# Kernel optimization log

Measured on AMD Instinct MI355X. Metric: run time of the kernel, lower is better.

## Reference

```python
import jax, jax.numpy as jnp
import numpy as np

D_MODEL = 1024
N_HEADS = 16
D_HEAD = D_MODEL // N_HEADS


def setup_inputs() -> dict:
    key = jax.random.key(0)
    ks = jax.random.split(key, 5)
    scale = 1.0 / np.sqrt(D_MODEL)
    return {
        "x": jax.random.normal(ks[0], (2, 2048, D_MODEL), dtype=jnp.float32),
        "W_q": jax.random.normal(ks[1], (D_MODEL, D_MODEL), dtype=jnp.float32) * scale,
        "W_k": jax.random.normal(ks[2], (D_MODEL, D_MODEL), dtype=jnp.float32) * scale,
        "W_v": jax.random.normal(ks[3], (D_MODEL, D_MODEL), dtype=jnp.float32) * scale,
        "W_o": jax.random.normal(ks[4], (D_MODEL, D_MODEL), dtype=jnp.float32) * scale,
    }


def reference(x, W_q, W_k, W_v, W_o):
    B, S, _ = x.shape
    # nn.Linear computes x @ W.T; weights stored [out, in]
    def proj(W):
        y = jnp.einsum("bsd,ed->bse", x, W)
        return y.reshape(B, S, N_HEADS, D_HEAD).transpose(0, 2, 1, 3)  # [B,H,S,Dh]

    q, k, v = proj(W_q), proj(W_k), proj(W_v)
    scores = jnp.einsum("bhqd,bhkd->bhqk", q, k) / jnp.sqrt(jnp.float32(D_HEAD))
    causal = jnp.triu(jnp.ones((S, S), dtype=bool), k=1)
    scores = jnp.where(causal, -jnp.inf, scores)
    attn = jax.nn.softmax(scores, axis=-1)
    out = jnp.einsum("bhqk,bhkd->bhqd", attn, v)  # [B,H,S,Dh]
    out = out.transpose(0, 2, 1, 3).reshape(B, S, D_MODEL)
    return jnp.einsum("bsd,ed->bse", out, W_o)
```

## Files before the change

### kernel.cpp

```cpp
#include <hip/hip_runtime.h>


#define DMODEL 1024
#define NHEADS 16
#define DHEAD  64
#define SEQ    2048
#define BATCH  2
#define MROWS  (BATCH * SEQ)

typedef __bf16 bf16x8 __attribute__((ext_vector_type(8)));
typedef __bf16 bf16x4 __attribute__((ext_vector_type(4)));
typedef float  f32x4  __attribute__((ext_vector_type(4)));

__device__ __forceinline__ f32x4 mfma16(bf16x8 a, bf16x8 b, f32x4 c) {
    return __builtin_amdgcn_mfma_f32_16x16x32_bf16(a, b, c, 0, 0, 0);
}

__device__ __forceinline__ bf16x8 ld8(const float* p) {
    const f32x4 a0 = *(const f32x4*)p;
    const f32x4 a1 = *(const f32x4*)(p + 4);
    bf16x8 v;
    v[0] = (__bf16)a0[0]; v[1] = (__bf16)a0[1];
    v[2] = (__bf16)a0[2]; v[3] = (__bf16)a0[3];
    v[4] = (__bf16)a1[0]; v[5] = (__bf16)a1[1];
    v[6] = (__bf16)a1[2]; v[7] = (__bf16)a1[3];
    return v;
}

__device__ __forceinline__ void gll16(const __bf16* g, __bf16* l) {
    __builtin_amdgcn_global_load_lds(
        (const __attribute__((address_space(1))) void*)g,
        (__attribute__((address_space(3))) void*)l,
        16, 0, 0);
}

__global__ __launch_bounds__(256) void cvt_kernel(const float* __restrict__ x,
                                                  const float* __restrict__ Wq,
                                                  const float* __restrict__ Wk,
                                                  const float* __restrict__ Wv,
                                                  const float* __restrict__ Wo,
                                                  __bf16* __restrict__ xb,
                                                  __bf16* __restrict__ wcat) {
    const int y = blockIdx.y;
    const float* src;
    __bf16* dst;
    int nchunks;
    if (y == 0) { src = x; dst = xb; nchunks = (MROWS * DMODEL) / 8; }
    else {
        src = (y == 1) ? Wq : (y == 2) ? Wk : (y == 3) ? Wv : Wo;
        dst = wcat + (size_t)(y - 1) * DMODEL * DMODEL;
        nchunks = (DMODEL * DMODEL) / 8;
    }
    const int c = blockIdx.x * 256 + threadIdx.x;
    if (c < nchunks) *(bf16x8*)(dst + (size_t)c * 8) = ld8(src + (size_t)c * 8);
}

template <typename TC>
__device__ __forceinline__ void gemm_bb_body(const __bf16* __restrict__ A,
                                             const __bf16* __restrict__ W,
                                             TC* __restrict__ C,
                                             __bf16* __restrict__ VT,
                                             bool vt, int m0, int n0,
                                             float scale) {
    constexpr int K = DMODEL;
    __shared__ __align__(16) __bf16 As[128][64];
    __shared__ __align__(16) __bf16 Bs[128][64];

    const int tid  = threadIdx.x;
    const int lane = tid & 63;
    const int wave = tid >> 6;
    const int quad = lane >> 4;
    const int l16  = lane & 15;
    const int wm   = wave & 1;
    const int wn   = wave >> 1;

    const int sr = lane >> 3;
    const int sc = ((lane & 7) ^ sr) * 8;

    f32x4 acc[4][4] = {};

    for (int k0 = 0; k0 < K; k0 += 64) {
        __syncthreads();
#pragma unroll
        for (int s = 0; s < 4; ++s) {
            const int row = s * 32 + wave * 8 + sr;
            gll16(A + (size_t)(m0 + row) * K + k0 + sc, &As[s * 32 + wave * 8][0]);
            gll16(W + (size_t)(n0 + row) * K + k0 + sc, &Bs[s * 32 + wave * 8][0]);
        }
        __syncthreads();

#pragma unroll
        for (int h = 0; h < 2; ++h) {
            bf16x8 af[4], bfr[4];
#pragma unroll
            for (int i = 0; i < 4; ++i) {
                const int gr = ((h * 4 + quad) ^ (l16 & 7)) * 8;
                af[i]  = *(const bf16x8*)(&As[wm * 64 + i * 16 + l16][gr]);
                bfr[i] = *(const bf16x8*)(&Bs[wn * 64 + i * 16 + l16][gr]);
            }
#pragma unroll
            for (int mi = 0; mi < 4; ++mi)
#pragma unroll
                for (int ni = 0; ni < 4; ++ni)
                    acc[mi][ni] = mfma16(af[mi], bfr[ni], acc[mi][ni]);
        }
    }

    if (!vt) {
#pragma unroll
        for (int mi = 0; mi < 4; ++mi)
#pragma unroll
            for (int ni = 0; ni < 4; ++ni)
#pragma unroll
                for (int r = 0; r < 4; ++r) {
                    int row = m0 + wm * 64 + mi * 16 + quad * 4 + r;
                    int col = n0 + wn * 64 + ni * 16 + l16;
                    C[(size_t)row * DMODEL + col] = (TC)(acc[mi][ni][r] * scale);
                }
    } else {
#pragma unroll
        for (int mi = 0; mi < 4; ++mi)
#pragma unroll
            for (int ni = 0; ni < 4; ++ni) {
                const int m  = m0 + wm * 64 + mi * 16 + quad * 4;
                const int hd = n0 + wn * 64 + ni * 16 + l16;
                bf16x4 v4;
#pragma unroll
                for (int r = 0; r < 4; ++r) v4[r] = (__bf16)acc[mi][ni][r];
                *(bf16x4*)(VT + (size_t)hd * MROWS + m) = v4;
            }
    }
}

#define QSCALE 0.1803368801111204f

__global__ __launch_bounds__(256) void qkv_kernel(const __bf16* __restrict__ X,
                                                  const __bf16* __restrict__ wcat,
                                                  __bf16* __restrict__ Q,
                                                  __bf16* __restrict__ K,
                                                  __bf16* __restrict__ VT) {
    const int z = blockIdx.z;
    const __bf16* W = wcat + (size_t)z * DMODEL * DMODEL;
    __bf16* Y = (z == 0) ? Q : K;
    const float scale = (z == 0) ? QSCALE : 1.0f;
    gemm_bb_body<__bf16>(X, W, Y, VT, z == 2,
                         blockIdx.y * 128, blockIdx.x * 128, scale);
}

__global__ __launch_bounds__(256) void out_gemm_kernel(const __bf16* __restrict__ A,
                                                       const __bf16* __restrict__ W,
                                                       float* __restrict__ C) {
    gemm_bb_body<float>(A, W, C, nullptr, false,
                        blockIdx.y * 128, blockIdx.x * 128, 1.0f);
}

__global__ __launch_bounds__(128) void attn_kernel(const __bf16* __restrict__ Q,
                                                   const __bf16* __restrict__ Kg,
                                                   const __bf16* __restrict__ VTg,
                                                   __bf16* __restrict__ O) {
    const int bh = blockIdx.x;
    const int qt = 63 - blockIdx.y;
    const int b = bh >> 4, h = bh & 15;
    const size_t base = (size_t)b * SEQ * DMODEL + (size_t)h * DHEAD;

    const int tid  = threadIdx.x;
    const int lane = tid & 63;
    const int wave = tid >> 6;
    const int quad = lane >> 4;
    const int l16  = lane & 15;

    __shared__ __align__(16) __bf16 Ks[32][64];
    __shared__ __align__(16) __bf16 Vs[64][32];
    __shared__ __align__(16) __bf16 Ps[2][16][40];

    const int ksr = lane >> 3;
    const int ksc = ((lane & 7) ^ ksr) * 8;
    const int vsr = lane >> 2;
    const int vsc = ((lane & 3) ^ ((lane >> 3) & 3)) * 8;

    const int qrow = qt * 32 + wave * 16 + l16;

    const bf16x8 qf0 = *(const bf16x8*)(Q + base + (size_t)qrow * DMODEL + quad * 8);
    const bf16x8 qf1 = *(const bf16x8*)(Q + base + (size_t)qrow * DMODEL + 32 + quad * 8);

    f32x4 oacc[4] = {};
    float m_i = -1e30f, l_i = 0.f;

    for (int kt = 0; kt <= qt; ++kt) {
        const int k0 = kt * 32;
        __syncthreads();
#pragma unroll
        for (int j = 0; j < 2; ++j) {
            gll16(Kg + base + (size_t)(k0 + wave * 16 + j * 8 + ksr) * DMODEL + ksc,
                  &Ks[wave * 16 + j * 8][0]);
            gll16(VTg + (size_t)(h * 64 + j * 32 + wave * 16 + vsr) * MROWS
                      + (size_t)b * SEQ + k0 + vsc,
                  &Vs[j * 32 + wave * 16][0]);
        }
        __syncthreads();

        const bool diag = (kt == qt);

        const int g0 = ((quad ^ (l16 & 7))) * 8;
        const int g1 = ((quad ^ 4) ^ (l16 & 7)) * 8;
        const bf16x8 kf00 = *(const bf16x8*)(&Ks[l16][g0]);
        const bf16x8 kf01 = *(const bf16x8*)(&Ks[l16][g1]);
        const bf16x8 kf10 = *(const bf16x8*)(&Ks[16 + l16][g0]);
        const bf16x8 kf11 = *(const bf16x8*)(&Ks[16 + l16][g1]);
        f32x4 s0 = {}, s1 = {};
        s0 = mfma16(kf00, qf0, s0); s0 = mfma16(kf01, qf1, s0);
        s1 = mfma16(kf10, qf0, s1); s1 = mfma16(kf11, qf1, s1);

        float mx;
        bool ok[2][4];
        if (!diag) {
            float m0 = s0[0];
#pragma unroll
            for (int r = 1; r < 4; ++r) m0 = fmaxf(m0, s0[r]);
#pragma unroll
            for (int r = 0; r < 4; ++r) m0 = fmaxf(m0, s1[r]);
            mx = m0;
        } else {
            mx = -1e30f;
#pragma unroll
            for (int hh = 0; hh < 2; ++hh)
#pragma unroll
                for (int r = 0; r < 4; ++r) {
                    const int kk = k0 + hh * 16 + quad * 4 + r;
                    ok[hh][r] = (kk <= qrow);
                    const float v = hh ? s1[r] : s0[r];
                    mx = fmaxf(mx, ok[hh][r] ? v : -1e30f);
                }
        }
        mx = fmaxf(mx, __shfl_xor(mx, 16));
        mx = fmaxf(mx, __shfl_xor(mx, 32));
        const float mnew  = fmaxf(m_i, mx);
        const float alpha = exp2f(m_i - mnew);
        m_i = mnew;

        float p[2][4];
        float rs = 0.f;
        if (!diag) {
#pragma unroll
            for (int hh = 0; hh < 2; ++hh)
#pragma unroll
                for (int r = 0; r < 4; ++r) {
                    p[hh][r] = exp2f((hh ? s1[r] : s0[r]) - mnew);
                    rs += p[hh][r];
                }
        } else {
#pragma unroll
            for (int hh = 0; hh < 2; ++hh)
#pragma unroll
                for (int r = 0; r < 4; ++r) {
                    p[hh][r] = ok[hh][r] ? exp2f((hh ? s1[r] : s0[r]) - mnew) : 0.f;
                    rs += p[hh][r];
                }
        }
        rs += __shfl_xor(rs, 16);
        rs += __shfl_xor(rs, 32);
        l_i = l_i * alpha + rs;

        bf16x4 w0, w1;
#pragma unroll
        for (int r = 0; r < 4; ++r) { w0[r] = (__bf16)p[0][r]; w1[r] = (__bf16)p[1][r]; }
        *(bf16x4*)(&Ps[wave][l16][quad * 4])      = w0;
        *(bf16x4*)(&Ps[wave][l16][16 + quad * 4]) = w1;

        const bf16x8 pf = *(const bf16x8*)(&Ps[wave][l16][quad * 8]);
        const int vg = (quad ^ ((l16 >> 1) & 3)) * 8;
#pragma unroll
        for (int f = 0; f < 4; ++f) {
            const bf16x8 vf = *(const bf16x8*)(&Vs[f * 16 + l16][vg]);
            oacc[f] = mfma16(vf, pf, oacc[f] * alpha);
        }
    }

    const float inv = (l_i > 0.f) ? (1.f / l_i) : 0.f;
#pragma unroll
    for (int f = 0; f < 4; ++f) {
        bf16x4 o;
#pragma unroll
        for (int r = 0; r < 4; ++r) o[r] = (__bf16)(oacc[f][r] * inv);
        *(bf16x4*)(O + base + (size_t)qrow * DMODEL + f * 16 + quad * 4) = o;
    }
}

extern "C" void kernel_launch(void* const* d_in, const int* in_sizes, int n_in,
                              void* d_out, int out_size, void* d_ws, size_t ws_size,
                              hipStream_t stream) {
    const float* x  = (const float*)d_in[0];
    const float* Wq = (const float*)d_in[1];
    const float* Wk = (const float*)d_in[2];
    const float* Wv = (const float*)d_in[3];
    const float* Wo = (const float*)d_in[4];
    float* out = (float*)d_out;

    const size_t tm = (size_t)MROWS * DMODEL;
    const size_t tw = (size_t)DMODEL * DMODEL;
    __bf16* Q    = (__bf16*)d_ws;
    __bf16* K    = Q + tm;
    __bf16* VT   = K + tm;
    __bf16* xb   = VT + tm;
    __bf16* wcat = xb + tm;

    dim3 gc(2048, 5);
    cvt_kernel<<<gc, 256, 0, stream>>>(x, Wq, Wk, Wv, Wo, xb, wcat);

    dim3 g1(DMODEL / 128, MROWS / 128, 3);
    qkv_kernel<<<g1, 256, 0, stream>>>(xb, wcat, Q, K, VT);

    dim3 g2(BATCH * NHEADS, SEQ / 32);
    attn_kernel<<<g2, 128, 0, stream>>>(Q, K, VT, Q);

    dim3 g3(DMODEL / 128, MROWS / 128);
    out_gemm_kernel<<<g3, 256, 0, stream>>>(Q, wcat + 3 * tw, out);
}
```

Baseline: 217.5 us.

## Widen attention KV tile to 64 keys and halve GEMM K-step to 32

The attention kernel now processes 64 keys per iteration using larger swizzled K/V shared tiles and two PV MFMAs per output fragment. This halves the number of loop iterations, barriers and online-softmax rescales per query tile. The projection GEMM drops its K-step from 64 to 32 with a simpler, unswizzled LDS layout. That shrinks shared memory use but doubles barrier count and may add LDS bank conflicts. The diagonal tile now masks up to 64 keys, so more masked work is wasted on even query tiles.

```diff
diff --git a/kernel.cpp b/kernel.cpp
--- a/kernel.cpp
+++ b/kernel.cpp
@@ -63,8 +63,8 @@
                                              bool vt, int m0, int n0,
                                              float scale) {
     constexpr int K = DMODEL;
-    __shared__ __align__(16) __bf16 As[128][64];
-    __shared__ __align__(16) __bf16 Bs[128][64];
+    __shared__ __align__(16) __bf16 As[128][32];
+    __shared__ __align__(16) __bf16 Bs[128][32];
 
     const int tid  = threadIdx.x;
     const int lane = tid & 63;
@@ -74,36 +74,35 @@
     const int wm   = wave & 1;
     const int wn   = wave >> 1;
 
-    const int sr = lane >> 3;
-    const int sc = ((lane & 7) ^ sr) * 8;
+    const int srow = lane >> 2;
+    const int scol = (lane & 3) * 8;
+
+    const __bf16* a0p = A + (size_t)(m0 + wave * 16 + srow) * K + scol;
+    const __bf16* a1p = A + (size_t)(m0 + 64 + wave * 16 + srow) * K + scol;
+    const __bf16* b0p = W + (size_t)(n0 + wave * 16 + srow) * K + scol;
+    const __bf16* b1p = W + (size_t)(n0 + 64 + wave * 16 + srow) * K + scol;
 
     f32x4 acc[4][4] = {};
 
-    for (int k0 = 0; k0 < K; k0 += 64) {
+    for (int k0 = 0; k0 < K; k0 += 32) {
         __syncthreads();
-#pragma unroll
-        for (int s = 0; s < 4; ++s) {
-            const int row = s * 32 + wave * 8 + sr;
-            gll16(A + (size_t)(m0 + row) * K + k0 + sc, &As[s * 32 + wave * 8][0]);
-            gll16(W + (size_t)(n0 + row) * K + k0 + sc, &Bs[s * 32 + wave * 8][0]);
-        }
+        gll16(a0p + k0, &As[wave * 16][0]);
+        gll16(a1p + k0, &As[64 + wave * 16][0]);
+        gll16(b0p + k0, &Bs[wave * 16][0]);
+        gll16(b1p + k0, &Bs[64 + wave * 16][0]);
         __syncthreads();
 
-#pragma unroll
-        for (int h = 0; h < 2; ++h) {
-            bf16x8 af[4], bfr[4];
-#pragma unroll
-            for (int i = 0; i < 4; ++i) {
-                const int gr = ((h * 4 + quad) ^ (l16 & 7)) * 8;
-                af[i]  = *(const bf16x8*)(&As[wm * 64 + i * 16 + l16][gr]);
-                bfr[i] = *(const bf16x8*)(&Bs[wn * 64 + i * 16 + l16][gr]);
-            }
-#pragma unroll
-            for (int mi = 0; mi < 4; ++mi)
-#pragma unroll
-                for (int ni = 0; ni < 4; ++ni)
-                    acc[mi][ni] = mfma16(af[mi], bfr[ni], acc[mi][ni]);
-        }
+        bf16x8 af[4], bfr[4];
+#pragma unroll
+        for (int i = 0; i < 4; ++i) {
+            af[i]  = *(const bf16x8*)(&As[wm * 64 + i * 16 + l16][quad * 8]);
+            bfr[i] = *(const bf16x8*)(&Bs[wn * 64 + i * 16 + l16][quad * 8]);
+        }
+#pragma unroll
+        for (int mi = 0; mi < 4; ++mi)
+#pragma unroll
+            for (int ni = 0; ni < 4; ++ni)
+                acc[mi][ni] = mfma16(af[mi], bfr[ni], acc[mi][ni]);
     }
 
     if (!vt) {
@@ -169,14 +168,12 @@
     const int quad = lane >> 4;
     const int l16  = lane & 15;
 
-    __shared__ __align__(16) __bf16 Ks[32][64];
-    __shared__ __align__(16) __bf16 Vs[64][32];
-    __shared__ __align__(16) __bf16 Ps[2][16][40];
-
-    const int ksr = lane >> 3;
-    const int ksc = ((lane & 7) ^ ksr) * 8;
-    const int vsr = lane >> 2;
-    const int vsc = ((lane & 3) ^ ((lane >> 3) & 3)) * 8;
+    __shared__ __align__(16) __bf16 Ks[64][64];
+    __shared__ __align__(16) __bf16 Vs[64][64];
+    __shared__ __align__(16) __bf16 Ps[2][2][16][40];
+
+    const int sr = lane >> 3;
+    const int sc = ((lane & 7) ^ sr) * 8;
 
     const int qrow = qt * 32 + wave * 16 + l16;
 
@@ -186,50 +183,51 @@
     f32x4 oacc[4] = {};
     float m_i = -1e30f, l_i = 0.f;
 
-    for (int kt = 0; kt <= qt; ++kt) {
-        const int k0 = kt * 32;
+    const int ntiles = (qt >> 1) + 1;
+    const int gsw = (l16 & 7);
+
+    for (int kt = 0; kt < ntiles; ++kt) {
+        const int k0 = kt * 64;
         __syncthreads();
 #pragma unroll
-        for (int j = 0; j < 2; ++j) {
-            gll16(Kg + base + (size_t)(k0 + wave * 16 + j * 8 + ksr) * DMODEL + ksc,
-                  &Ks[wave * 16 + j * 8][0]);
-            gll16(VTg + (size_t)(h * 64 + j * 32 + wave * 16 + vsr) * MROWS
-                      + (size_t)b * SEQ + k0 + vsc,
-                  &Vs[j * 32 + wave * 16][0]);
+        for (int j = 0; j < 4; ++j) {
+            const int row = wave * 32 + j * 8;
+            gll16(Kg + base + (size_t)(k0 + row + sr) * DMODEL + sc, &Ks[row][0]);
+            gll16(VTg + (size_t)(h * 64 + row + sr) * MROWS + (size_t)b * SEQ + k0 + sc,
+                  &Vs[row][0]);
         }
         __syncthreads();
 
-        const bool diag = (kt == qt);
-
-        const int g0 = ((quad ^ (l16 & 7))) * 8;
-        const int g1 = ((quad ^ 4) ^ (l16 & 7)) * 8;
-        const bf16x8 kf00 = *(const bf16x8*)(&Ks[l16][g0]);
-        const bf16x8 kf01 = *(const bf16x8*)(&Ks[l16][g1]);
-        const bf16x8 kf10 = *(const bf16x8*)(&Ks[16 + l16][g0]);
-        const bf16x8 kf11 = *(const bf16x8*)(&Ks[16 + l16][g1]);
-        f32x4 s0 = {}, s1 = {};
-        s0 = mfma16(kf00, qf0, s0); s0 = mfma16(kf01, qf1, s0);
-        s1 = mfma16(kf10, qf0, s1); s1 = mfma16(kf11, qf1, s1);
+        const bool diag = (kt == ntiles - 1);
+
+        f32x4 s[4];
+#pragma unroll
+        for (int g = 0; g < 4; ++g) {
+            const bf16x8 kfa = *(const bf16x8*)(&Ks[g * 16 + l16][(quad ^ gsw) * 8]);
+            const bf16x8 kfb = *(const bf16x8*)(&Ks[g * 16 + l16][((quad + 4) ^ gsw) * 8]);
+            f32x4 t = {};
+            t = mfma16(kfa, qf0, t);
+            t = mfma16(kfb, qf1, t);
+            s[g] = t;
+        }
 
         float mx;
-        bool ok[2][4];
+        bool ok[4][4];
         if (!diag) {
-            float m0 = s0[0];
-#pragma unroll
-            for (int r = 1; r < 4; ++r) m0 = fmaxf(m0, s0[r]);
-#pragma unroll
-            for (int r = 0; r < 4; ++r) m0 = fmaxf(m0, s1[r]);
-            mx = m0;
+            mx = s[0][0];
+#pragma unroll
+            for (int g = 0; g < 4; ++g)
+#pragma unroll
+                for (int r = 0; r < 4; ++r) mx = fmaxf(mx, s[g][r]);
         } else {
             mx = -1e30f;
 #pragma unroll
-            for (int hh = 0; hh < 2; ++hh)
+            for (int g = 0; g < 4; ++g)
 #pragma unroll
                 for (int r = 0; r < 4; ++r) {
-                    const int kk = k0 + hh * 16 + quad * 4 + r;
-                    ok[hh][r] = (kk <= qrow);
-                    const float v = hh ? s1[r] : s0[r];
-                    mx = fmaxf(mx, ok[hh][r] ? v : -1e30f);
+                    const int kk = k0 + g * 16 + quad * 4 + r;
+                    ok[g][r] = (kk <= qrow);
+                    mx = fmaxf(mx, ok[g][r] ? s[g][r] : -1e30f);
                 }
         }
         mx = fmaxf(mx, __shfl_xor(mx, 16));
@@ -238,41 +236,45 @@
         const float alpha = exp2f(m_i - mnew);
         m_i = mnew;
 
-        float p[2][4];
         float rs = 0.f;
+        bf16x4 w4[4];
         if (!diag) {
 #pragma unroll
-            for (int hh = 0; hh < 2; ++hh)
+            for (int g = 0; g < 4; ++g)
 #pragma unroll
                 for (int r = 0; r < 4; ++r) {
-                    p[hh][r] = exp2f((hh ? s1[r] : s0[r]) - mnew);
-                    rs += p[hh][r];
+                    const float p = exp2f(s[g][r] - mnew);
+                    rs += p;
+                    w4[g][r] = (__bf16)p;
                 }
         } else {
 #pragma unroll
-            for (int hh = 0; hh < 2; ++hh)
+            for (int g = 0; g < 4; ++g)
 #pragma unroll
                 for (int r = 0; r < 4; ++r) {
-                    p[hh][r] = ok[hh][r] ? exp2f((hh ? s1[r] : s0[r]) - mnew) : 0.f;
-                    rs += p[hh][r];
+                    const float p = ok[g][r] ? exp2f(s[g][r] - mnew) : 0.f;
+                    rs += p;
+                    w4[g][r] = (__bf16)p;
                 }
         }
         rs += __shfl_xor(rs, 16);
         rs += __shfl_xor(rs, 32);
         l_i = l_i * alpha + rs;
 
-        bf16x4 w0, w1;
-#pragma unroll
-        for (int r = 0; r < 4; ++r) { w0[r] = (__bf16)p[0][r]; w1[r] = (__bf16)p[1][r]; }
-        *(bf16x4*)(&Ps[wave][l16][quad * 4])      = w0;
-        *(bf16x4*)(&Ps[wave][l16][16 + quad * 4]) = w1;
-
-        const bf16x8 pf = *(const bf16x8*)(&Ps[wave][l16][quad * 8]);
-        const int vg = (quad ^ ((l16 >> 1) & 3)) * 8;
+#pragma unroll
+        for (int g = 0; g < 4; ++g)
+            *(bf16x4*)(&Ps[wave][g >> 1][l16][(g & 1) * 16 + quad * 4]) = w4[g];
+
+        const bf16x8 pf0 = *(const bf16x8*)(&Ps[wave][0][l16][quad * 8]);
+        const bf16x8 pf1 = *(const bf16x8*)(&Ps[wave][1][l16][quad * 8]);
 #pragma unroll
         for (int f = 0; f < 4; ++f) {
-            const bf16x8 vf = *(const bf16x8*)(&Vs[f * 16 + l16][vg]);
-            oacc[f] = mfma16(vf, pf, oacc[f] * alpha);
+            const bf16x8 vfa = *(const bf16x8*)(&Vs[f * 16 + l16][(quad ^ gsw) * 8]);
+            const bf16x8 vfb = *(const bf16x8*)(&Vs[f * 16 + l16][((quad + 4) ^ gsw) * 8]);
+            f32x4 t = oacc[f] * alpha;
+            t = mfma16(vfa, pf0, t);
+            t = mfma16(vfb, pf1, t);
+            oacc[f] = t;
         }
     }
 
```

New measurement: 194.5 us. -10.6%, faster.
